# Kernel optimization log

Measured on AMD Instinct MI355X. Metric: run time of the kernel, lower is better.

## Reference

```python
import jax, jax.numpy as jnp
import numpy as np

B, N, PH = 256, 21, 12
FEAT, INP, LAT, HID, OUT, NT = 8, 256, 64, 512, 128, 4
IN0 = FEAT + LAT + INP  # 328: GRU / initial-hidden input width


def _l1norm(G):
    # torch.nn.functional.normalize(G, p=1, dim=1)
    return G / jnp.maximum(jnp.abs(G).sum(axis=1, keepdims=True), 1e-12)


def _graph_linear(x, G, W, b, T):
    # StaticGraphLinear with learn_influence=True: y = G_l1norm @ (x @ W[T]^T + b)
    y = jnp.einsum('bni,noi->bno', x, W[T]) + b
    return jnp.einsum('nm,bmo->bno', _l1norm(G), y)


def _quat_exp(v):
    # Quaternion(angle=|v|, axis=v).q -> [cos(t/2), sin(t/2)*v/|v|]
    theta = jnp.linalg.norm(v, axis=-1, keepdims=True)
    w = jnp.cos(0.5 * theta)
    k = jnp.where(theta > 1e-8, jnp.sin(0.5 * theta) / jnp.maximum(theta, 1e-8), 0.5)
    return jnp.concatenate([w, k * v], axis=-1)


def _qmul(a, b):
    # Hamilton product a*b, w-first convention
    w1, v1 = a[..., :1], a[..., 1:]
    w2, v2 = b[..., :1], b[..., 1:]
    w = w1 * w2 - jnp.sum(v1 * v2, axis=-1, keepdims=True)
    v = w1 * v2 + w2 * v1 + jnp.cross(v1, v2)
    return jnp.concatenate([w, v], axis=-1)


def setup_inputs() -> dict:
    key = jax.random.key(0)
    ks = jax.random.split(key, 26)
    s = 0.05
    eyeN = jnp.eye(N, dtype=jnp.float32)
    inp = {}
    inp['x'] = jax.random.normal(ks[0], (B, 2, N, FEAT), dtype=jnp.float32)
    inp['h'] = jax.random.normal(ks[1], (B, N, INP), dtype=jnp.float32)
    inp['z'] = jax.random.normal(ks[2], (B, N, LAT), dtype=jnp.float32)
    q = jax.random.normal(ks[3], (B, N, 4), dtype=jnp.float32)
    inp['q_t'] = q / jnp.linalg.norm(q, axis=-1, keepdims=True)
    inp['T'] = jax.random.randint(ks[4], (N,), 0, NT)
    inp['ph'] = PH
    # initial_hidden_h
    inp['W0'] = s * jax.random.normal(ks[5], (NT, HID, IN0))
    inp['b0'] = s * jax.random.normal(ks[6], (N, HID))
    inp['G0'] = eyeN + s * jax.random.normal(ks[7], (N, N))
    # StaticGraphGRU (1 layer)
    inp['Wih'] = s * jax.random.normal(ks[8], (NT, 3 * HID, IN0))
    inp['Whh'] = s * jax.random.normal(ks[9], (NT, 3 * HID, HID))
    inp['bih'] = s * jax.random.normal(ks[10], (N, 3 * HID))
    inp['bhh'] = s * jax.random.normal(ks[11], (N, 3 * HID))
    inp['Grnn'] = eyeN + s * jax.random.normal(ks[12], (N, N))
    inp['GA'] = s * jax.random.normal(ks[13], (N, N))  # learned additive influence
    # fc_q / fc_cov_lat
    inp['Wq'] = s * jax.random.normal(ks[14], (NT, OUT, HID))
    inp['bq'] = s * jax.random.normal(ks[15], (N, OUT))
    inp['Gq'] = eyeN + s * jax.random.normal(ks[16], (N, N))
    inp['Wc'] = s * jax.random.normal(ks[17], (NT, OUT, HID))
    inp['bc'] = s * jax.random.normal(ks[18], (N, OUT))
    inp['Gc'] = eyeN + s * jax.random.normal(ks[19], (N, N))
    # to_q / to_q_cov_lat (learn_influence=False -> identity influence)
    inp['W3'] = s * jax.random.normal(ks[20], (NT, 3, OUT))
    inp['b3'] = s * jax.random.normal(ks[21], (N, 3))
    inp['W6'] = s * jax.random.normal(ks[22], (NT, 6, OUT))
    inp['b6'] = s * jax.random.normal(ks[23], (N, 6))
    return inp


def reference(x, h, z, q_t, T, ph, W0, b0, G0, Wih, Whh, bih, bhh, Grnn, GA,
              Wq, bq, Gq, Wc, bc, Gc, W3, b3, W6, b6):
    x_t = x[:, -1]    # [B,N,FEAT]
    x_t_1 = x[:, -2]
    h_z = jnp.concatenate([z, h], axis=-1)  # [B,N,LAT+INP]
    rnn_h = _graph_linear(jnp.concatenate([x_t_1, h_z], axis=-1), G0, W0, b0, T)
    Gn = _l1norm(Grnn) + GA           # additive graph influence
    WihT, WhhT = Wih[T], Whh[T]       # gather per-node weights once [N,3H,*]
    W3T, W6T = W3[T], W6[T]

    def step(carry, _):
        x_c, q_c, h_c = carry
        xin = jnp.concatenate([x_c, h_z], axis=-1)  # [B,N,IN0]
        xr = jnp.einsum('nm,bmg->bng', Gn, jnp.einsum('bni,ngi->bng', xin, WihT) + bih)
        hr = jnp.einsum('nm,bmg->bng', Gn, jnp.einsum('bnh,ngh->bng', h_c, WhhT) + bhh)
        ir, iz, ic = jnp.split(xr, 3, axis=-1)
        hrr, hz2, hc2 = jnp.split(hr, 3, axis=-1)
        r = jax.nn.sigmoid(ir + hrr)
        zg = jax.nn.sigmoid(iz + hz2)
        n = jnp.tanh(ic + r * hc2)
        h_new = (1.0 - zg) * n + zg * h_c
        y = jnp.tanh(h_new)  # dropout=0 (eval)
        ys = jnp.tanh(_graph_linear(y, Gq, Wq, bq, T))
        yc = jnp.tanh(_graph_linear(y, Gc, Wc, bc, T))
        dq3 = jnp.einsum('bno,nao->bna', ys, W3T) + b3
        cov = jnp.einsum('bno,nao->bna', yc, W6T) + b6
        dq = _quat_exp(dq3)
        q_new = _qmul(dq, q_c)
        x_new = jnp.concatenate([q_new, dq], axis=-1)
        return (x_new, q_new, h_new), (dq, cov)

    _, (dqs, covs) = jax.lax.scan(step, (x_t, q_t, rnn_h), None, length=ph)
    dq = jnp.moveaxis(dqs, 0, 1)        # [B,ph,N,4]
    dq_cov_lat = jnp.moveaxis(covs, 0, 1)  # [B,ph,N,6]
    return dq, dq_cov_lat, x_t  # (dp, dp_cov_lat are None since position=False)
```

## Files before the change

kernel.cpp:

```cpp
#include <hip/hip_runtime.h>

typedef unsigned short u16;
typedef __bf16 bf16_t;
typedef bf16_t bf16x8 __attribute__((ext_vector_type(8)));
typedef float f32x4 __attribute__((ext_vector_type(4)));
typedef long long i64;

#define NN   21
#define BB   256
#define HID  512
#define G3   1536
#define NC2  2048
#define A0S  352
#define PH   12
#define WSK  516
#define LK   40
#define KP   544

__device__ __forceinline__ u16 f2b(float f){ bf16_t b = (bf16_t)f; return __builtin_bit_cast(u16, b); }
__device__ __forceinline__ float b2f(u16 u){ bf16_t b = __builtin_bit_cast(bf16_t, u); return (float)b; }
__device__ __forceinline__ bf16_t fb(float f){ return (bf16_t)f; }
__device__ __forceinline__ float sigm(float x){ return 1.0f / (1.0f + __expf(-x)); }
__device__ __forceinline__ float ftanh(float x){
  x = fminf(15.0f, fmaxf(-15.0f, x));
  float e = __expf(2.0f * x);
  return (e - 1.0f) / (e + 1.0f);
}
__device__ __forceinline__ float ldf(const void* p, size_t idx, int mode){
  if (mode == 2) return b2f(((const u16*)p)[idx]);
  if (mode == 1) return (float)((const double*)p)[idx];
  return ((const float*)p)[idx];
}

__global__ void k_fill(float* out, int n, float c){
  int idx = blockIdx.x*256 + threadIdx.x;
  if (idx < n) out[idx] = c;
}

__global__ void k_detect(const void* w0raw, const void* traw, int* flags){
  if (threadIdx.x != 0 || blockIdx.x != 0) return;
  const float*  v32 = (const float*)w0raw;
  const double* v64 = (const double*)w0raw;
  const u16*    vbf = (const u16*)w0raw;
  int c32 = 0, c64 = 0, cbf = 0;
  for (int i = 0; i < 64; ++i){
    float a32 = fabsf(v32[i]);
    if (a32 >= 1e-8f && a32 <= 1e4f) ++c32;
    double a64 = fabs(v64[i]);
    if (a64 >= 1e-8 && a64 <= 1e4) ++c64;
    float abf = fabsf(b2f(vbf[i]));
    if (abf >= 1e-8f && abf <= 1e4f) ++cbf;
  }
  int mode;
  if (cbf >= 60 && c32 < 48) mode = 2;
  else if (c32 >= 48)        mode = 0;
  else if (c64 >= 48)        mode = 1;
  else                       mode = 2;
  flags[0] = mode;
  const int* tw = (const int*)traw;
  int ok64 = 1;
  for (int i = 0; i < NN; ++i){
    unsigned lo = (unsigned)tw[2*i];
    int hi = tw[2*i+1];
    if (hi != 0 || lo >= 4u) { ok64 = 0; break; }
  }
  flags[1] = ok64;
}
__global__ void k_cvt_i(const void* src, int* dst, int n, const int* flags){
  int idx = threadIdx.x;
  if (idx >= n) return;
  if (flags[1]) dst[idx] = (int)((const i64*)src)[idx];
  else          dst[idx] = ((const int*)src)[idx];
}
__global__ void k_cvt_f(const void* src, float* dst, int n, const int* flags){
  int idx = blockIdx.x*256 + threadIdx.x;
  if (idx < n) dst[idx] = ldf(src, idx, flags[0]);
}
__global__ void k_cvt_wpadg(const void* W, u16* dst, int rows, int srcK, int dstK, const int* flags){
  int idx = blockIdx.x*256 + threadIdx.x;
  if (idx >= rows*dstK) return;
  int k = idx % dstK, r = idx / dstK;
  dst[idx] = (k < srcK) ? f2b(ldf(W, (size_t)r*srcK + k, flags[0])) : (u16)0;
}
__global__ void k_cvt_w(const void* W, u16* dst, int n, const int* flags){
  int idx = blockIdx.x*256 + threadIdx.x;
  if (idx < n) dst[idx] = f2b(ldf(W, idx, flags[0]));
}
__global__ void k_cvt_wstat(const void* Wih, u16* dst, const int* flags){
  int idx = blockIdx.x*256 + threadIdx.x;
  if (idx >= 4*G3*320) return;
  int k2 = idx % 320, tg = idx / 320;
  dst[idx] = f2b(ldf(Wih, (size_t)tg*328 + 8 + k2, flags[0]));
}
__global__ void k_pack_wpack(const void* Whh, const void* Wih, u16* Wp, const int* flags){
  int idx = blockIdx.x*256 + threadIdx.x;
  if (idx >= 4*NC2*KP) return;
  const int md = flags[0];
  int k  = idx % KP;
  int tg = idx / KP;
  int g  = tg % NC2;
  int t  = tg / NC2;
  float v = 0.f;
  if (g < 1024){
    if (k < 512)             v = ldf(Whh, ((size_t)(t*G3 + g) << 9) + k, md);
    else if (k < 520)        v = ldf(Wih, (size_t)(t*G3 + g)*328 + (k - 512), md);
  } else if (g < 1536){
    if (k >= 512 && k < 520) v = ldf(Wih, (size_t)(t*G3 + g)*328 + (k - 512), md);
  } else {
    if (k < 512)             v = ldf(Whh, ((size_t)(t*G3 + (g - 512)) << 9) + k, md);
  }
  Wp[idx] = f2b(v);
}
__global__ void k_cvt_wqc(const void* Wq, const void* Wc, u16* dst, const int* flags){
  int idx = blockIdx.x*256 + threadIdx.x;
  if (idx >= 4*256*512) return;
  int k  = idx & 511;
  int tg = idx >> 9;
  int g  = tg & 255;
  int t  = tg >> 8;
  const int md = flags[0];
  dst[idx] = f2b((g < 128) ? ldf(Wq, ((size_t)(t*128 + g) << 9) + k, md)
                           : ldf(Wc, ((size_t)(t*128 + (g-128)) << 9) + k, md));
}
__global__ void k_bqc(const void* bq, const void* bc, float* bqc, const int* flags){
  int idx = blockIdx.x*256 + threadIdx.x;
  if (idx >= NN*256) return;
  int o = idx & 255; int n = idx >> 8;
  const int md = flags[0];
  bqc[idx] = (o < 128) ? ldf(bq,(size_t)n*128+o,md) : ldf(bc,(size_t)n*128+(o-128),md);
}
__global__ void k_biasS(const void* bih, const void* bhh, float* biasS, float* bhh2, const int* flags){
  int idx = blockIdx.x*256 + threadIdx.x;
  if (idx >= NN*G3) return;
  const int md = flags[0];
  int g = idx % G3;
  float v = ldf(bih, idx, md);
  if (g < 1024) v += ldf(bhh, idx, md);
  biasS[idx] = v;
  if (g >= 1024){
    int n = idx / G3;
    bhh2[n*512 + (g - 1024)] = ldf(bhh, idx, md);
  }
}

__global__ void k_prep_G(const void* G0, const void* Grnn, const void* GA,
                         const void* Gq, const void* Gc, const int* flags,
                         float* G0s, float* Gns, float* Gqs, float* Gcs){
  int tid = threadIdx.x;
  if (tid >= 84) return;
  const int md = flags[0];
  int mat = tid / 21, row = tid % 21;
  const void* src = mat==0 ? G0 : mat==1 ? Grnn : mat==2 ? Gq : Gc;
  float* dst      = mat==0 ? G0s : mat==1 ? Gns : mat==2 ? Gqs : Gcs;
  float s = 0.f;
  for (int m=0;m<21;++m) s += fabsf(ldf(src,row*21+m,md));
  s = fmaxf(s, 1e-12f);
  for (int m=0;m<21;++m){
    float v = ldf(src,row*21+m,md) / s;
    if (mat==1) v += ldf(GA,row*21+m,md);
    dst[row*21+m] = v;
  }
}

__global__ void k_build_A0(const void* x, const void* z, const void* hin,
                           const int* flags, u16* A0){
  int idx = blockIdx.x*256 + threadIdx.x;
  if (idx >= NN*BB*A0S) return;
  const int md = flags[0];
  int k  = idx % A0S;
  int nb = idx / A0S;
  int b  = nb % BB;
  int n  = nb / BB;
  float v = 0.f;
  if (k < 8)        v = ldf(x, ((size_t)(b*2 + 0)*NN + n)*8 + k, md);
  else if (k < 72)  v = ldf(z, ((size_t)b*NN + n)*64 + (k - 8), md);
  else if (k < 328) v = ldf(hin, ((size_t)b*NN + n)*256 + (k - 72), md);
  A0[idx] = f2b(v);
}

__global__ void k_init_state(const void* x, const void* qt, const int* flags,
                             u16* Axin, float* qc, float* out2){
  int b = threadIdx.x; int n = blockIdx.x;
  const int md = flags[0];
  for (int f=0; f<8; ++f){
    float raw = ldf(x, ((size_t)(b*2 + 1)*NN + n)*8 + f, md);
    Axin[(size_t)(n*BB + b)*A0S + f] = f2b(raw);
    out2[(b*NN + n)*8 + f] = raw;
  }
  for (int c=0; c<4; ++c) qc[(n*BB + b)*4 + c] = ldf(qt, ((size_t)b*NN + n)*4 + c, md);
}

template<int ABF>
__global__ __launch_bounds__(256)
void k_ngemm(const void* __restrict__ A_, int sA,
             const void* __restrict__ W_, int sW, size_t tstride,
             const void* __restrict__ bias_, int biasN,
             const int* __restrict__ T, const int* __restrict__ flags, int K,
             float* __restrict__ C, int Nc)
{
  __shared__ float Ws[8*WSK];
  const int node = blockIdx.y;
  const int g0   = blockIdx.x*8;
  const int tid  = threadIdx.x;
  const int t    = T[node];
  const int md   = flags[0];
  for (int idx = tid; idx < 8*K; idx += 256){
    int gg = idx / K, kk = idx - gg*K;
    Ws[gg*WSK + kk] = ldf(W_, (size_t)t*tstride + (size_t)(g0+gg)*sW + kk, md);
  }
  __syncthreads();
  const int b = tid;
  const float* Af = (const float*)A_;
  const u16*   Ab = (const u16*)A_;
  float acc[8];
  #pragma unroll
  for (int gg=0; gg<8; ++gg) acc[gg] = ldf(bias_, (size_t)node*biasN + g0 + gg, md);
  const size_t abase = (size_t)(node*BB + b)*sA;
  for (int k=0; k<K; ++k){
    const float av = ABF ? b2f(Ab[abase + k]) : Af[abase + k];
    #pragma unroll
    for (int gg=0; gg<8; ++gg) acc[gg] += av * Ws[gg*WSK + k];
  }
  #pragma unroll
  for (int gg=0; gg<8; ++gg)
    C[(size_t)(node*BB + b)*Nc + g0 + gg] = acc[gg];
}

template<int AMODE, int GRUH, int FOUT>
__global__ __launch_bounds__(256,2)
void k_mgemm(const void* __restrict__ A_, int sA,
             const u16* __restrict__ W, int sW, size_t tstride,
             const int* __restrict__ T, int nchunks,
             const float* __restrict__ bias, int biasN,
             void* __restrict__ C_, int Nc, int goff)
{
  __shared__ u16 As[128*LK];
  __shared__ u16 Bs[128*LK];
  const int ntile = blockIdx.x, mtile = blockIdx.y, node = blockIdx.z;
  const int tid = threadIdx.x;
  const int t = T[node];
  const int lane = tid & 63, wv = tid >> 6;
  const int wm = wv & 1, wn = wv >> 1;
  const int l16 = lane & 15, quad = lane >> 4;
  const int row0 = mtile*128, col0 = ntile*128;
  u16* Cb = (u16*)C_;
  float* Cf = (float*)C_;

  f32x4 acc[4][4];
  #pragma unroll
  for (int mt=0; mt<4; ++mt)
  #pragma unroll
  for (int nt=0; nt<4; ++nt){
    const int col = col0 + wn*64 + nt*16 + l16;
    const float bv = bias[node*biasN + col];
    if (GRUH && ntile < 8){
      #pragma unroll
      for (int r=0;r<4;++r){
        const int row = row0 + wm*64 + mt*16 + quad*4 + r;
        acc[mt][nt][r] = bv + b2f(Cb[(size_t)(node*BB + row)*Nc + col]);
      }
    } else {
      #pragma unroll
      for (int r=0;r<4;++r) acc[mt][nt][r] = bv;
    }
  }

  const int sr = tid >> 1, seg = tid & 1;
  for (int kc = 0; kc < nchunks; ++kc){
    const int k0 = kc*32 + seg*16;
    if (AMODE == 0){
      const u16* srcA = (const u16*)A_ + (size_t)(node*BB + row0 + sr)*sA + k0;
      *(uint4*)&As[sr*LK + seg*16]     = *(const uint4*)srcA;
      *(uint4*)&As[sr*LK + seg*16 + 8] = *(const uint4*)(srcA + 8);
    } else {
      const float* srcA = (const float*)A_ + (size_t)(node*BB + row0 + sr)*sA + k0;
      float4 f0 = *(const float4*)(srcA);
      float4 f1 = *(const float4*)(srcA+4);
      float4 f2 = *(const float4*)(srcA+8);
      float4 f3 = *(const float4*)(srcA+12);
      bf16x8 v0, v1;
      v0[0]=fb(f0.x); v0[1]=fb(f0.y); v0[2]=fb(f0.z); v0[3]=fb(f0.w);
      v0[4]=fb(f1.x); v0[5]=fb(f1.y); v0[6]=fb(f1.z); v0[7]=fb(f1.w);
      v1[0]=fb(f2.x); v1[1]=fb(f2.y); v1[2]=fb(f2.z); v1[3]=fb(f2.w);
      v1[4]=fb(f3.x); v1[5]=fb(f3.y); v1[6]=fb(f3.z); v1[7]=fb(f3.w);
      *(bf16x8*)&As[sr*LK + seg*16]     = v0;
      *(bf16x8*)&As[sr*LK + seg*16 + 8] = v1;
    }
    {
      const u16* srcB = W + (size_t)t*tstride + (size_t)(col0 + sr)*sW + k0;
      *(uint4*)&Bs[sr*LK + seg*16]     = *(const uint4*)srcB;
      *(uint4*)&Bs[sr*LK + seg*16 + 8] = *(const uint4*)(srcB + 8);
    }
    __syncthreads();
    bf16x8 af[4], bfr[4];
    #pragma unroll
    for (int mt=0; mt<4; ++mt) af[mt]  = *(const bf16x8*)&As[(wm*64 + mt*16 + l16)*LK + quad*8];
    #pragma unroll
    for (int nt=0; nt<4; ++nt) bfr[nt] = *(const bf16x8*)&Bs[(wn*64 + nt*16 + l16)*LK + quad*8];
    #pragma unroll
    for (int mt=0; mt<4; ++mt)
    #pragma unroll
    for (int nt=0; nt<4; ++nt)
      acc[mt][nt] = __builtin_amdgcn_mfma_f32_16x16x32_bf16(af[mt], bfr[nt], acc[mt][nt], 0, 0, 0);
    __syncthreads();
  }

  #pragma unroll
  for (int mt=0; mt<4; ++mt)
  #pragma unroll
  for (int nt=0; nt<4; ++nt){
    const int col = col0 + wn*64 + nt*16 + l16;
    const int dcol = GRUH ? ((ntile < 8) ? col : col + 512) : col + goff;
    #pragma unroll
    for (int r=0;r<4;++r){
      const int row = row0 + wm*64 + mt*16 + quad*4 + r;
      if (FOUT) Cf[(size_t)(node*BB + row)*Nc + dcol] = acc[mt][nt][r];
      else      Cb[(size_t)(node*BB + row)*Nc + dcol] = f2b(acc[mt][nt][r]);
    }
  }
}

__global__ __launch_bounds__(256,2)
void k_fgemm(const float* __restrict__ H, const u16* __restrict__ Ax,
             const u16* __restrict__ Wp,
             const int* __restrict__ T,
             const u16* __restrict__ Sbuf, const float* __restrict__ bhh2,
             u16* __restrict__ C)
{
  __shared__ u16 As[128*LK];
  __shared__ u16 Bs[128*LK];
  const int ntile = blockIdx.x, mtile = blockIdx.y, node = blockIdx.z;
  const int tid = threadIdx.x;
  const int t = T[node];
  const int lane = tid & 63, wv = tid >> 6;
  const int wm = wv & 1, wn = wv >> 1;
  const int l16 = lane & 15, quad = lane >> 4;
  const int row0 = mtile*128, col0 = ntile*128;

  f32x4 acc[4][4];
  #pragma unroll
  for (int mt=0; mt<4; ++mt)
  #pragma unroll
  for (int nt=0; nt<4; ++nt){
    const int col = col0 + wn*64 + nt*16 + l16;
    #pragma unroll
    for (int r=0;r<4;++r){
      const int row = row0 + wm*64 + mt*16 + quad*4 + r;
      acc[mt][nt][r] = (col < 1536)
        ? b2f(Sbuf[(size_t)(node*BB + row)*G3 + col])
        : bhh2[node*512 + (col - 1536)];
    }
  }

  int kc0 = 0, kc1 = 17;
  if (ntile >= 8 && ntile < 12) kc0 = 16;
  else if (ntile >= 12)         kc1 = 16;

  const int sr = tid >> 1, seg = tid & 1;
  for (int kc = kc0; kc < kc1; ++kc){
    const int k0 = kc*32 + seg*16;
    if (kc < 16){
      const float* srcA = H + (size_t)(node*BB + row0 + sr)*HID + k0;
      float4 f0 = *(const float4*)(srcA);
      float4 f1 = *(const float4*)(srcA+4);
      float4 f2 = *(const float4*)(srcA+8);
      float4 f3 = *(const float4*)(srcA+12);
      bf16x8 v0, v1;
      v0[0]=fb(f0.x); v0[1]=fb(f0.y); v0[2]=fb(f0.z); v0[3]=fb(f0.w);
      v0[4]=fb(f1.x); v0[5]=fb(f1.y); v0[6]=fb(f1.z); v0[7]=fb(f1.w);
      v1[0]=fb(f2.x); v1[1]=fb(f2.y); v1[2]=fb(f2.z); v1[3]=fb(f2.w);
      v1[4]=fb(f3.x); v1[5]=fb(f3.y); v1[6]=fb(f3.z); v1[7]=fb(f3.w);
      *(bf16x8*)&As[sr*LK + seg*16]     = v0;
      *(bf16x8*)&As[sr*LK + seg*16 + 8] = v1;
    } else {
      uint4 zz; zz.x = zz.y = zz.z = zz.w = 0u;
      uint4 u0 = zz;
      if (seg == 0) u0 = *(const uint4*)(Ax + (size_t)(node*BB + row0 + sr)*A0S);
      *(uint4*)&As[sr*LK + seg*16]     = u0;
      *(uint4*)&As[sr*LK + seg*16 + 8] = zz;
    }
    {
      const u16* srcB = Wp + (size_t)t*NC2*KP + (size_t)(col0 + sr)*KP + k0;
      *(uint4*)&Bs[sr*LK + seg*16]     = *(const uint4*)srcB;
      *(uint4*)&Bs[sr*LK + seg*16 + 8] = *(const uint4*)(srcB + 8);
    }
    __syncthreads();
    bf16x8 af[4], bfr[4];
    #pragma unroll
    for (int mt=0; mt<4; ++mt) af[mt]  = *(const bf16x8*)&As[(wm*64 + mt*16 + l16)*LK + quad*8];
    #pragma unroll
    for (int nt=0; nt<4; ++nt) bfr[nt] = *(const bf16x8*)&Bs[(wn*64 + nt*16 + l16)*LK + quad*8];
    #pragma unroll
    for (int mt=0; mt<4; ++mt)
    #pragma unroll
    for (int nt=0; nt<4; ++nt)
      acc[mt][nt] = __builtin_amdgcn_mfma_f32_16x16x32_bf16(af[mt], bfr[nt], acc[mt][nt], 0, 0, 0);
    __syncthreads();
  }

  #pragma unroll
  for (int mt=0; mt<4; ++mt)
  #pragma unroll
  for (int nt=0; nt<4; ++nt){
    const int col = col0 + wn*64 + nt*16 + l16;
    #pragma unroll
    for (int r=0;r<4;++r){
      const int row = row0 + wm*64 + mt*16 + quad*4 + r;
      C[(size_t)(node*BB + row)*NC2 + col] = f2b(acc[mt][nt][r]);
    }
  }
}


__global__ __launch_bounds__(256)
void k_mix_init(const float* C0, const float* G0s, float* h){
  __shared__ float Gs[441];
  const int tid = threadIdx.x;
  for (int i = tid; i < 441; i += 256) Gs[i] = G0s[i];
  __syncthreads();
  const int b = blockIdx.y;
  const int j = blockIdx.x*256 + tid;
  float P[21];
  #pragma unroll
  for (int m=0;m<21;++m) P[m] = C0[(size_t)(m*BB + b)*HID + j];
  float R[21];
  for (int n=0;n<21;++n){
    float s = 0.f;
    #pragma unroll
    for (int m=0;m<21;++m) s += Gs[n*21+m]*P[m];
    R[n] = s;
  }
  for (int n=0;n<21;++n) h[(size_t)(n*BB + b)*HID + j] = R[n];
}

__global__ __launch_bounds__(256)
void k_gru(u16* __restrict__ Cb, const float* __restrict__ Gns, float* __restrict__ h){
  __shared__ float Gs[441];
  const int tid = threadIdx.x;
  for (int i = tid; i < 441; i += 256) Gs[i] = Gns[i];
  __syncthreads();
  const int b = blockIdx.y;
  const int j = blockIdx.x*256 + tid;
  float P1[21], P2[21], P3[21], P4[21];
  #pragma unroll
  for (int m=0;m<21;++m){
    const size_t base = (size_t)(m*BB + b)*NC2 + j;
    P1[m] = b2f(Cb[base]);
    P2[m] = b2f(Cb[base + 512]);
    P3[m] = b2f(Cb[base + 1024]);
    P4[m] = b2f(Cb[base + 1536]);
  }
  for (int n=0;n<21;++n){
    float s1=0.f, s2=0.f, s3=0.f, s4=0.f;
    #pragma unroll
    for (int m=0;m<21;++m){
      const float g = Gs[n*21+m];
      s1 += g*P1[m]; s2 += g*P2[m]; s3 += g*P3[m]; s4 += g*P4[m];
    }
    const size_t hi = (size_t)(n*BB + b)*HID + j;
    const float hc = h[hi];
    const float r  = sigm(s1);
    const float zg = sigm(s2);
    const float nn = ftanh(s3 + r*s4);
    const float hn = (1.f - zg)*nn + zg*hc;
    h[hi] = hn;
    Cb[(size_t)(n*BB + b)*NC2 + j] = f2b(ftanh(hn));
  }
}

__global__ __launch_bounds__(256)
void k_out(const u16* __restrict__ Cbig, const float* __restrict__ Gqs, const float* __restrict__ Gcs,
           const int* __restrict__ T, const int* __restrict__ flags,
           const void* __restrict__ W3, const void* __restrict__ b3,
           const void* __restrict__ W6, const void* __restrict__ b6,
           float* __restrict__ qc, u16* __restrict__ Axin,
           float* __restrict__ out_dq, float* __restrict__ out_cov, int s)
{
  const int tid = threadIdx.x;
  const int w = blockIdx.x*4 + (tid >> 6);
  const int lane = tid & 63;
  const int b = w / 21, n = w % 21;
  const int t = T[n];
  const int md = flags[0];
  float aq1=0.f, aq2=0.f, ac1=0.f, ac2=0.f;
  #pragma unroll
  for (int m=0;m<21;++m){
    const u16* c = Cbig + (size_t)(m*BB + b)*NC2 + 512;
    const float gq = Gqs[n*21+m], gc = Gcs[n*21+m];
    aq1 += gq*b2f(c[lane]);       aq2 += gq*b2f(c[lane+64]);
    ac1 += gc*b2f(c[lane+128]);   ac2 += gc*b2f(c[lane+192]);
  }
  const float ys1 = ftanh(aq1), ys2 = ftanh(aq2);
  const float yc1 = ftanh(ac1), yc2 = ftanh(ac2);
  float red[9];
  #pragma unroll
  for (int a=0;a<3;++a)
    red[a] = ys1*ldf(W3,(size_t)(t*3+a)*128 + lane,md) + ys2*ldf(W3,(size_t)(t*3+a)*128 + lane + 64,md);
  #pragma unroll
  for (int a=0;a<6;++a)
    red[3+a] = yc1*ldf(W6,(size_t)(t*6+a)*128 + lane,md) + yc2*ldf(W6,(size_t)(t*6+a)*128 + lane + 64,md);
  #pragma unroll
  for (int i=0;i<9;++i){
    red[i] += __shfl_xor(red[i], 32);
    red[i] += __shfl_xor(red[i], 16);
    red[i] += __shfl_xor(red[i], 8);
    red[i] += __shfl_xor(red[i], 4);
    red[i] += __shfl_xor(red[i], 2);
    red[i] += __shfl_xor(red[i], 1);
  }
  const float d0 = red[0] + ldf(b3,(size_t)n*3+0,md);
  const float d1 = red[1] + ldf(b3,(size_t)n*3+1,md);
  const float d2 = red[2] + ldf(b3,(size_t)n*3+2,md);
  const float theta = sqrtf(d0*d0 + d1*d1 + d2*d2);
  const float wq = cosf(0.5f*theta);
  const float kq = (theta > 1e-8f) ? (sinf(0.5f*theta) / fmaxf(theta, 1e-8f)) : 0.5f;
  const float x1 = kq*d0, y1 = kq*d1, z1 = kq*d2;
  if (lane == 0){
    float* q = qc + (size_t)(n*BB + b)*4;
    const float qw=q[0], qx=q[1], qy=q[2], qz=q[3];
    const float nw = wq*qw - (x1*qx + y1*qy + z1*qz);
    const float nx = wq*qx + qw*x1 + (y1*qz - z1*qy);
    const float ny = wq*qy + qw*y1 + (z1*qx - x1*qz);
    const float nz = wq*qz + qw*z1 + (x1*qy - y1*qx);
    q[0]=nw; q[1]=nx; q[2]=ny; q[3]=nz;
    u16* ax = Axin + (size_t)(n*BB + b)*A0S;
    ax[0]=f2b(nw); ax[1]=f2b(nx); ax[2]=f2b(ny); ax[3]=f2b(nz);
    ax[4]=f2b(wq); ax[5]=f2b(x1); ax[6]=f2b(y1); ax[7]=f2b(z1);
    float* od = out_dq + (size_t)((b*PH + s)*NN + n)*4;
    od[0]=wq; od[1]=x1; od[2]=y1; od[3]=z1;
    float* oc = out_cov + (size_t)((b*PH + s)*NN + n)*6;
    for (int a=0;a<6;++a) oc[a] = red[3+a] + ldf(b6,(size_t)n*6+a,md);
  }
}


extern "C" void kernel_launch(void* const* d_in, const int* in_sizes, int n_in,
                              void* d_out, int out_size, void* d_ws, size_t ws_size,
                              hipStream_t stream)
{
  const void* P[25];
  {
    int j = 0;
    for (int i = 0; i < 25; ++i){
      if (i == 5){ P[i] = nullptr; continue; }
      while (j < n_in && in_sizes[j] == 1) ++j;
      P[i] = (j < n_in) ? d_in[j++] : nullptr;
    }
  }

  float* out_dq  = (float*)d_out;
  float* out_cov = out_dq  + (size_t)BB*PH*NN*4;
  float* out_xt  = out_cov + (size_t)BB*PH*NN*6;

  char* wsb = (char*)d_ws;
  size_t off = 0;
  auto carve = [&](size_t bytes)->void*{
    void* p = wsb + off;
    off = (off + bytes + 255) & ~(size_t)255;
    return p;
  };

  int*   flags = (int*)  carve(2*4);
  int*   TI    = (int*)  carve(NN*4);
  float* G0s   = (float*)carve(441*4);
  float* Gns   = (float*)carve(441*4);
  float* Gqs   = (float*)carve(441*4);
  float* Gcs   = (float*)carve(441*4);
  float* bqcF  = (float*)carve((size_t)NN*256*4);
  float* qcv   = (float*)carve((size_t)NN*BB*4*4);
  u16*   Axin  = (u16*)  carve((size_t)NN*BB*A0S*2);
  u16*   Wqcb  = (u16*)  carve((size_t)4*256*512*2);
  float* hbuf  = (float*)carve((size_t)NN*BB*HID*4);
  u16*   Cbig  = (u16*)  carve((size_t)NN*BB*NC2*2);
  const size_t COMMON = off;

  size_t offA = off;
  auto carveA = [&](size_t bytes)->void*{
    void* p = wsb + offA;
    offA = (offA + bytes + 255) & ~(size_t)255;
    return p;
  };
  float* b0F   = (float*)carveA((size_t)NN*HID*4);
  float* biasS = (float*)carveA((size_t)NN*G3*4);
  float* bhh2F = (float*)carveA((size_t)NN*512*4);
  u16*   W0b   = (u16*)  carveA((size_t)4*HID*A0S*2);
  u16*   Wstat = (u16*)  carveA((size_t)4*G3*320*2);
  u16*   Wpack = (u16*)  carveA((size_t)4*NC2*KP*2);
  u16*   Sbuf  = (u16*)  carveA((size_t)NN*BB*G3*2);
  const size_t NEED_A = offA;

  size_t offB = off;
  auto carveB = [&](size_t bytes)->void*{
    void* p = wsb + offB;
    offB = (offB + bytes + 255) & ~(size_t)255;
    return p;
  };
  float* bihF  = (float*)carveB((size_t)NN*G3*4);
  float* bhhF  = (float*)carveB((size_t)NN*G3*4);
  u16*   Wihb  = (u16*)  carveB((size_t)4*G3*A0S*2);
  u16*   Whhb  = (u16*)  carveB((size_t)4*G3*512*2);
  const size_t NEED_B = offB;

  if (ws_size < NEED_B){
    float code = 150.0f + (float)(ws_size >> 23);
    k_fill<<<(out_size+255)/256,256,0,stream>>>((float*)d_out, out_size, code);
    return;
  }
  (void)COMMON;

  k_detect<<<1,64,0,stream>>>(P[6], P[4], flags);
  k_cvt_i<<<1,64,0,stream>>>(P[4], TI, NN, flags);
  k_prep_G<<<1,128,0,stream>>>(P[8],P[13],P[14],P[17],P[20],flags, G0s,Gns,Gqs,Gcs);
  k_bqc<<<(NN*256+255)/256,256,0,stream>>>(P[16],P[19],bqcF,flags);
  k_build_A0<<<(NN*BB*A0S+255)/256,256,0,stream>>>(P[0],P[2],P[1],flags,Axin);
  k_cvt_wqc<<<(4*256*512+255)/256,256,0,stream>>>(P[15],P[18],Wqcb,flags);

  if (ws_size >= NEED_A){
    k_cvt_f<<<(NN*HID+255)/256,256,0,stream>>>(P[7], b0F, NN*HID, flags);
    k_biasS<<<(NN*G3+255)/256,256,0,stream>>>(P[11],P[12],biasS,bhh2F,flags);
    k_cvt_wpadg<<<(4*HID*A0S+255)/256,256,0,stream>>>(P[6], W0b, 4*HID, 328, A0S, flags);
    k_cvt_wstat<<<(4*G3*320+255)/256,256,0,stream>>>(P[9], Wstat, flags);
    k_pack_wpack<<<(4*NC2*KP+255)/256,256,0,stream>>>(P[10], P[9], Wpack, flags);

    k_mgemm<0,0,1><<<dim3(4,2,NN),256,0,stream>>>(Axin,A0S, W0b,A0S,(size_t)HID*A0S,
        TI, 11, b0F,HID, hbuf,HID, 0);
    k_mix_init<<<dim3(2,BB),256,0,stream>>>(hbuf,G0s,hbuf);
    k_mgemm<0,0,0><<<dim3(12,2,NN),256,0,stream>>>(Axin+8,A0S, Wstat,320,(size_t)G3*320,
        TI, 10, biasS,G3, Sbuf,G3, 0);
    k_init_state<<<NN,256,0,stream>>>(P[0],P[3],flags,Axin,qcv,out_xt);

    for (int s=0; s<PH; ++s){
      k_fgemm<<<dim3(16,2,NN),256,0,stream>>>(hbuf,Axin,Wpack,TI,Sbuf,bhh2F,Cbig);
      k_gru<<<dim3(2,BB),256,0,stream>>>(Cbig,Gns,hbuf);
      k_mgemm<0,0,0><<<dim3(2,2,NN),256,0,stream>>>(Cbig,NC2, Wqcb,512,(size_t)256*512,
          TI, 16, bqcF,256, Cbig,NC2, 512);
      k_out<<<(NN*BB)/4,256,0,stream>>>(Cbig,Gqs,Gcs,TI,flags,P[21],P[22],P[23],P[24],
          qcv,Axin,out_dq,out_cov,s);
    }
  } else {
    k_cvt_f<<<(NN*G3+255)/256,256,0,stream>>>(P[11], bihF, NN*G3, flags);
    k_cvt_f<<<(NN*G3+255)/256,256,0,stream>>>(P[12], bhhF, NN*G3, flags);
    k_cvt_wpadg<<<(4*G3*A0S+255)/256,256,0,stream>>>(P[9], Wihb, 4*G3, 328, A0S, flags);
    k_cvt_w<<<(4*G3*512+255)/256,256,0,stream>>>(P[10], Whhb, 4*G3*512, flags);

    k_ngemm<1><<<dim3(HID/8,NN),256,0,stream>>>(Axin,A0S, P[6],328,(size_t)512*328,
        P[7],512, TI,flags, 328, hbuf,512);
    k_mix_init<<<dim3(2,BB),256,0,stream>>>(hbuf,G0s,hbuf);
    k_init_state<<<NN,256,0,stream>>>(P[0],P[3],flags,Axin,qcv,out_xt);

    for (int s=0; s<PH; ++s){
      k_mgemm<0,0,0><<<dim3(12,2,NN),256,0,stream>>>(Axin,A0S, Wihb,A0S,(size_t)G3*A0S,
          TI, 11, bihF,G3, Cbig,NC2, 0);
      k_mgemm<1,1,0><<<dim3(12,2,NN),256,0,stream>>>(hbuf,HID, Whhb,512,(size_t)G3*512,
          TI, 16, bhhF,G3, Cbig,NC2, 0);
      k_gru<<<dim3(2,BB),256,0,stream>>>(Cbig,Gns,hbuf);
      k_mgemm<0,0,0><<<dim3(2,2,NN),256,0,stream>>>(Cbig,NC2, Wqcb,512,(size_t)256*512,
          TI, 16, bqcF,256, Cbig,NC2, 512);
      k_out<<<(NN*BB)/4,256,0,stream>>>(Cbig,Gqs,Gcs,TI,flags,P[21],P[22],P[23],P[24],
          qcv,Axin,out_dq,out_cov,s);
    }
  }
}
```

Baseline: 1.318 ms.

## Store GRU hidden state in bf16 and halve GEMM M-tiles to 64 rows

The recurrent hidden state is now kept in bf16 instead of fp32, so the fused GEMM loads it directly without per-element conversion and the GRU kernel reads and writes half the bytes. The GEMMs switch to 64-row M tiles with 4 blocks per CU launch bounds, doubling grid size for better occupancy across CUs. The initial projection writes fp32 into a scratch region reused from Cbig before mixing. This trades precision in the carried hidden state, which may accumulate rounding error over the steps, for lower memory traffic and more parallelism.

```diff
diff --git a/kernel.cpp b/kernel.cpp
--- a/kernel.cpp
+++ b/kernel.cpp
@@ -320,14 +320,15 @@
   }
 }
 
-__global__ __launch_bounds__(256,2)
-void k_fgemm(const float* __restrict__ H, const u16* __restrict__ Ax,
-             const u16* __restrict__ Wp,
-             const int* __restrict__ T,
-             const u16* __restrict__ Sbuf, const float* __restrict__ bhh2,
-             u16* __restrict__ C)
+template<int FOUT>
+__global__ __launch_bounds__(256,4)
+void k_tg(const u16* __restrict__ A, int sA,
+          const u16* __restrict__ W, int sW, size_t tstride,
+          const int* __restrict__ T, int nchunks,
+          const float* __restrict__ bias, int biasN,
+          void* __restrict__ C_, int Nc, int goff)
 {
-  __shared__ u16 As[128*LK];
+  __shared__ u16 As[64*LK];
   __shared__ u16 Bs[128*LK];
   const int ntile = blockIdx.x, mtile = blockIdx.y, node = blockIdx.z;
   const int tid = threadIdx.x;
@@ -335,17 +336,82 @@
   const int lane = tid & 63, wv = tid >> 6;
   const int wm = wv & 1, wn = wv >> 1;
   const int l16 = lane & 15, quad = lane >> 4;
-  const int row0 = mtile*128, col0 = ntile*128;
-
-  f32x4 acc[4][4];
-  #pragma unroll
-  for (int mt=0; mt<4; ++mt)
+  const int row0 = mtile*64, col0 = ntile*128;
+  u16* Cb = (u16*)C_; float* Cf = (float*)C_;
+
+  f32x4 acc[2][4];
+  #pragma unroll
+  for (int mt=0; mt<2; ++mt)
+  #pragma unroll
+  for (int nt=0; nt<4; ++nt){
+    const float bv = bias[node*biasN + col0 + wn*64 + nt*16 + l16];
+    #pragma unroll
+    for (int r=0;r<4;++r) acc[mt][nt][r] = bv;
+  }
+
+  const int arow = tid >> 2, aseg = tid & 3;
+  const int brow = tid >> 1, bseg = tid & 1;
+  for (int kc = 0; kc < nchunks; ++kc){
+    *(uint4*)&As[arow*LK + aseg*8] =
+      *(const uint4*)(A + (size_t)(node*BB + row0 + arow)*sA + kc*32 + aseg*8);
+    {
+      const u16* srcB = W + (size_t)t*tstride + (size_t)(col0 + brow)*sW + kc*32 + bseg*16;
+      *(uint4*)&Bs[brow*LK + bseg*16]     = *(const uint4*)srcB;
+      *(uint4*)&Bs[brow*LK + bseg*16 + 8] = *(const uint4*)(srcB + 8);
+    }
+    __syncthreads();
+    bf16x8 af[2], bfr[4];
+    #pragma unroll
+    for (int mt=0; mt<2; ++mt) af[mt]  = *(const bf16x8*)&As[(wm*32 + mt*16 + l16)*LK + quad*8];
+    #pragma unroll
+    for (int nt=0; nt<4; ++nt) bfr[nt] = *(const bf16x8*)&Bs[(wn*64 + nt*16 + l16)*LK + quad*8];
+    #pragma unroll
+    for (int mt=0; mt<2; ++mt)
+    #pragma unroll
+    for (int nt=0; nt<4; ++nt)
+      acc[mt][nt] = __builtin_amdgcn_mfma_f32_16x16x32_bf16(af[mt], bfr[nt], acc[mt][nt], 0, 0, 0);
+    __syncthreads();
+  }
+
+  #pragma unroll
+  for (int mt=0; mt<2; ++mt)
+  #pragma unroll
+  for (int nt=0; nt<4; ++nt){
+    const int col = col0 + wn*64 + nt*16 + l16 + goff;
+    #pragma unroll
+    for (int r=0;r<4;++r){
+      const int row = row0 + wm*32 + mt*16 + quad*4 + r;
+      if (FOUT) Cf[(size_t)(node*BB + row)*Nc + col] = acc[mt][nt][r];
+      else      Cb[(size_t)(node*BB + row)*Nc + col] = f2b(acc[mt][nt][r]);
+    }
+  }
+}
+
+__global__ __launch_bounds__(256,4)
+void k_fg(const u16* __restrict__ hb, const u16* __restrict__ Ax,
+          const u16* __restrict__ Wp, const int* __restrict__ T,
+          const u16* __restrict__ Sbuf, const float* __restrict__ bhh2,
+          u16* __restrict__ C)
+{
+  __shared__ u16 As[64*LK];
+  __shared__ u16 Bs[128*LK];
+  const int ntile = blockIdx.x, mtile = blockIdx.y, node = blockIdx.z;
+  const int tid = threadIdx.x;
+  const int t = T[node];
+  const int lane = tid & 63, wv = tid >> 6;
+  const int wm = wv & 1, wn = wv >> 1;
+  const int l16 = lane & 15, quad = lane >> 4;
+  const int row0 = mtile*64, col0 = ntile*128;
+
+  f32x4 acc[2][4];
+  #pragma unroll
+  for (int mt=0; mt<2; ++mt)
   #pragma unroll
   for (int nt=0; nt<4; ++nt){
     const int col = col0 + wn*64 + nt*16 + l16;
     #pragma unroll
     for (int r=0;r<4;++r){
-      const int row = row0 + wm*64 + mt*16 + quad*4 + r;
+      const int row = row0 + wm*32 + mt*16 + quad*4 + r;
       acc[mt][nt][r] = (col < 1536)
         ? b2f(Sbuf[(size_t)(node*BB + row)*G3 + col])
         : bhh2[node*512 + (col - 1536)];
@@ -356,42 +422,31 @@
   if (ntile >= 8 && ntile < 12) kc0 = 16;
   else if (ntile >= 12)         kc1 = 16;
 
-  const int sr = tid >> 1, seg = tid & 1;
+  const int arow = tid >> 2, aseg = tid & 3;
+  const int brow = tid >> 1, bseg = tid & 1;
   for (int kc = kc0; kc < kc1; ++kc){
-    const int k0 = kc*32 + seg*16;
     if (kc < 16){
-      const float* srcA = H + (size_t)(node*BB + row0 + sr)*HID + k0;
-      float4 f0 = *(const float4*)(srcA);
-      float4 f1 = *(const float4*)(srcA+4);
-      float4 f2 = *(const float4*)(srcA+8);
-      float4 f3 = *(const float4*)(srcA+12);
-      bf16x8 v0, v1;
-      v0[0]=fb(f0.x); v0[1]=fb(f0.y); v0[2]=fb(f0.z); v0[3]=fb(f0.w);
-      v0[4]=fb(f1.x); v0[5]=fb(f1.y); v0[6]=fb(f1.z); v0[7]=fb(f1.w);
-      v1[0]=fb(f2.x); v1[1]=fb(f2.y); v1[2]=fb(f2.z); v1[3]=fb(f2.w);
-      v1[4]=fb(f3.x); v1[5]=fb(f3.y); v1[6]=fb(f3.z); v1[7]=fb(f3.w);
-      *(bf16x8*)&As[sr*LK + seg*16]     = v0;
-      *(bf16x8*)&As[sr*LK + seg*16 + 8] = v1;
+      *(uint4*)&As[arow*LK + aseg*8] =
+        *(const uint4*)(hb + (size_t)(node*BB + row0 + arow)*HID + kc*32 + aseg*8);
     } else {
       uint4 zz; zz.x = zz.y = zz.z = zz.w = 0u;
       uint4 u0 = zz;
-      if (seg == 0) u0 = *(const uint4*)(Ax + (size_t)(node*BB + row0 + sr)*A0S);
-      *(uint4*)&As[sr*LK + seg*16]     = u0;
-      *(uint4*)&As[sr*LK + seg*16 + 8] = zz;
+      if (aseg == 0) u0 = *(const uint4*)(Ax + (size_t)(node*BB + row0 + arow)*A0S);
+      *(uint4*)&As[arow*LK + aseg*8] = u0;
     }
     {
-      const u16* srcB = Wp + (size_t)t*NC2*KP + (size_t)(col0 + sr)*KP + k0;
-      *(uint4*)&Bs[sr*LK + seg*16]     = *(const uint4*)srcB;
-      *(uint4*)&Bs[sr*LK + seg*16 + 8] = *(const uint4*)(srcB + 8);
+      const u16* srcB = Wp + (size_t)t*NC2*KP + (size_t)(col0 + brow)*KP + kc*32 + bseg*16;
+      *(uint4*)&Bs[brow*LK + bseg*16]     = *(const uint4*)srcB;
+      *(uint4*)&Bs[brow*LK + bseg*16 + 8] = *(const uint4*)(srcB + 8);
     }
     __syncthreads();
-    bf16x8 af[4], bfr[4];
-    #pragma unroll
-    for (int mt=0; mt<4; ++mt) af[mt]  = *(const bf16x8*)&As[(wm*64 + mt*16 + l16)*LK + quad*8];
+    bf16x8 af[2], bfr[4];
+    #pragma unroll
+    for (int mt=0; mt<2; ++mt) af[mt]  = *(const bf16x8*)&As[(wm*32 + mt*16 + l16)*LK + quad*8];
     #pragma unroll
     for (int nt=0; nt<4; ++nt) bfr[nt] = *(const bf16x8*)&Bs[(wn*64 + nt*16 + l16)*LK + quad*8];
     #pragma unroll
-    for (int mt=0; mt<4; ++mt)
+    for (int mt=0; mt<2; ++mt)
     #pragma unroll
     for (int nt=0; nt<4; ++nt)
       acc[mt][nt] = __builtin_amdgcn_mfma_f32_16x16x32_bf16(af[mt], bfr[nt], acc[mt][nt], 0, 0, 0);
@@ -399,21 +454,22 @@
   }
 
   #pragma unroll
-  for (int mt=0; mt<4; ++mt)
+  for (int mt=0; mt<2; ++mt)
   #pragma unroll
   for (int nt=0; nt<4; ++nt){
     const int col = col0 + wn*64 + nt*16 + l16;
     #pragma unroll
     for (int r=0;r<4;++r){
-      const int row = row0 + wm*64 + mt*16 + quad*4 + r;
+      const int row = row0 + wm*32 + mt*16 + quad*4 + r;
       C[(size_t)(node*BB + row)*NC2 + col] = f2b(acc[mt][nt][r]);
     }
   }
 }
 
 
+template<int HB>
 __global__ __launch_bounds__(256)
-void k_mix_init(const float* C0, const float* G0s, float* h){
+void k_mix_init(const float* C0, const float* G0s, void* h_){
   __shared__ float Gs[441];
   const int tid = threadIdx.x;
   for (int i = tid; i < 441; i += 256) Gs[i] = G0s[i];
@@ -430,11 +486,16 @@
     for (int m=0;m<21;++m) s += Gs[n*21+m]*P[m];
     R[n] = s;
   }
-  for (int n=0;n<21;++n) h[(size_t)(n*BB + b)*HID + j] = R[n];
-}
-
+  for (int n=0;n<21;++n){
+    const size_t hi = (size_t)(n*BB + b)*HID + j;
+    if (HB) ((u16*)h_)[hi] = f2b(R[n]);
+    else    ((float*)h_)[hi] = R[n];
+  }
+}
+
+template<int HB>
 __global__ __launch_bounds__(256)
-void k_gru(u16* __restrict__ Cb, const float* __restrict__ Gns, float* __restrict__ h){
+void k_gru(u16* __restrict__ Cb, const float* __restrict__ Gns, void* __restrict__ h_){
   __shared__ float Gs[441];
   const int tid = threadIdx.x;
   for (int i = tid; i < 441; i += 256) Gs[i] = Gns[i];
@@ -458,12 +519,13 @@
       s1 += g*P1[m]; s2 += g*P2[m]; s3 += g*P3[m]; s4 += g*P4[m];
     }
     const size_t hi = (size_t)(n*BB + b)*HID + j;
-    const float hc = h[hi];
+    const float hc = HB ? b2f(((u16*)h_)[hi]) : ((float*)h_)[hi];
     const float r  = sigm(s1);
     const float zg = sigm(s2);
     const float nn = ftanh(s3 + r*s4);
     const float hn = (1.f - zg)*nn + zg*hc;
-    h[hi] = hn;
+    if (HB) ((u16*)h_)[hi] = f2b(hn);
+    else    ((float*)h_)[hi] = hn;
     Cb[(size_t)(n*BB + b)*NC2 + j] = f2b(ftanh(hn));
   }
 }
@@ -572,7 +634,6 @@
   u16*   Wqcb  = (u16*)  carve((size_t)4*256*512*2);
   float* hbuf  = (float*)carve((size_t)NN*BB*HID*4);
   u16*   Cbig  = (u16*)  carve((size_t)NN*BB*NC2*2);
-  const size_t COMMON = off;
 
   size_t offA = off;
   auto carveA = [&](size_t bytes)->void*{
@@ -606,7 +667,6 @@
     k_fill<<<(out_size+255)/256,256,0,stream>>>((float*)d_out, out_size, code);
     return;
   }
-  (void)COMMON;
 
   k_detect<<<1,64,0,stream>>>(P[6], P[4], flags);
   k_cvt_i<<<1,64,0,stream>>>(P[4], TI, NN, flags);
@@ -616,23 +676,26 @@
   k_cvt_wqc<<<(4*256*512+255)/256,256,0,stream>>>(P[15],P[18],Wqcb,flags);
 
   if (ws_size >= NEED_A){
+    u16* hb = (u16*)hbuf;
+    float* C0f = (float*)Cbig;
+
     k_cvt_f<<<(NN*HID+255)/256,256,0,stream>>>(P[7], b0F, NN*HID, flags);
     k_biasS<<<(NN*G3+255)/256,256,0,stream>>>(P[11],P[12],biasS,bhh2F,flags);
     k_cvt_wpadg<<<(4*HID*A0S+255)/256,256,0,stream>>>(P[6], W0b, 4*HID, 328, A0S, flags);
     k_cvt_wstat<<<(4*G3*320+255)/256,256,0,stream>>>(P[9], Wstat, flags);
     k_pack_wpack<<<(4*NC2*KP+255)/256,256,0,stream>>>(P[10], P[9], Wpack, flags);
 
-    k_mgemm<0,0,1><<<dim3(4,2,NN),256,0,stream>>>(Axin,A0S, W0b,A0S,(size_t)HID*A0S,
-        TI, 11, b0F,HID, hbuf,HID, 0);
-    k_mix_init<<<dim3(2,BB),256,0,stream>>>(hbuf,G0s,hbuf);
-    k_mgemm<0,0,0><<<dim3(12,2,NN),256,0,stream>>>(Axin+8,A0S, Wstat,320,(size_t)G3*320,
+    k_tg<1><<<dim3(4,4,NN),256,0,stream>>>(Axin,A0S, W0b,A0S,(size_t)HID*A0S,
+        TI, 11, b0F,HID, C0f,HID, 0);
+    k_mix_init<1><<<dim3(2,BB),256,0,stream>>>(C0f,G0s,hb);
+    k_tg<0><<<dim3(12,4,NN),256,0,stream>>>(Axin+8,A0S, Wstat,320,(size_t)G3*320,
         TI, 10, biasS,G3, Sbuf,G3, 0);
     k_init_state<<<NN,256,0,stream>>>(P[0],P[3],flags,Axin,qcv,out_xt);
 
     for (int s=0; s<PH; ++s){
-      k_fgemm<<<dim3(16,2,NN),256,0,stream>>>(hbuf,Axin,Wpack,TI,Sbuf,bhh2F,Cbig);
-      k_gru<<<dim3(2,BB),256,0,stream>>>(Cbig,Gns,hbuf);
-      k_mgemm<0,0,0><<<dim3(2,2,NN),256,0,stream>>>(Cbig,NC2, Wqcb,512,(size_t)256*512,
+      k_fg<<<dim3(16,4,NN),256,0,stream>>>(hb,Axin,Wpack,TI,Sbuf,bhh2F,Cbig);
+      k_gru<1><<<dim3(2,BB),256,0,stream>>>(Cbig,Gns,hb);
+      k_tg<0><<<dim3(2,4,NN),256,0,stream>>>(Cbig,NC2, Wqcb,512,(size_t)256*512,
           TI, 16, bqcF,256, Cbig,NC2, 512);
       k_out<<<(NN*BB)/4,256,0,stream>>>(Cbig,Gqs,Gcs,TI,flags,P[21],P[22],P[23],P[24],
           qcv,Axin,out_dq,out_cov,s);
@@ -645,7 +708,7 @@
 
     k_ngemm<1><<<dim3(HID/8,NN),256,0,stream>>>(Axin,A0S, P[6],328,(size_t)512*328,
         P[7],512, TI,flags, 328, hbuf,512);
-    k_mix_init<<<dim3(2,BB),256,0,stream>>>(hbuf,G0s,hbuf);
+    k_mix_init<0><<<dim3(2,BB),256,0,stream>>>(hbuf,G0s,hbuf);
     k_init_state<<<NN,256,0,stream>>>(P[0],P[3],flags,Axin,qcv,out_xt);
 
     for (int s=0; s<PH; ++s){
@@ -653,7 +716,7 @@
           TI, 11, bihF,G3, Cbig,NC2, 0);
       k_mgemm<1,1,0><<<dim3(12,2,NN),256,0,stream>>>(hbuf,HID, Whhb,512,(size_t)G3*512,
           TI, 16, bhhF,G3, Cbig,NC2, 0);
-      k_gru<<<dim3(2,BB),256,0,stream>>>(Cbig,Gns,hbuf);
+      k_gru<0><<<dim3(2,BB),256,0,stream>>>(Cbig,Gns,hbuf);
       k_mgemm<0,0,0><<<dim3(2,2,NN),256,0,stream>>>(Cbig,NC2, Wqcb,512,(size_t)256*512,
           TI, 16, bqcF,256, Cbig,NC2, 512);
       k_out<<<(NN*BB)/4,256,0,stream>>>(Cbig,Gqs,Gcs,TI,flags,P[21],P[22],P[23],P[24],
```

Result: faster. 1.155 ms (-12.3%).
